# Performance work log

Measured on AMD Instinct MI355X. Metric: run time of the kernel, lower is better.

## Reference

```python
import jax, jax.numpy as jnp
import numpy as np

BITS = 4
QMAX = (1 << BITS) - 1      # 15
QHALF = 1 << (BITS - 1)     # 8
B, S = 4, 2048
IN, OUT, FP = 4096, 4096, 256
INT = IN - FP


def setup_inputs() -> dict:
    key = jax.random.key(0)
    k0, k1, k2, k3 = jax.random.split(key, 4)
    x = jax.random.normal(k0, (B, S, IN), dtype=jnp.float16)
    # disjoint outlier / int feature index sets (QUIK splits columns by outlier-ness)
    perm = np.random.default_rng(0).permutation(IN)
    fp_indices = jnp.sort(jnp.asarray(perm[:FP], dtype=jnp.int32))
    int_indices = jnp.sort(jnp.asarray(perm[FP:], dtype=jnp.int32))
    # unpacked int4 weight values in [-8, 7] (torch stores these packed 2-per-uint8)
    int_weight = jax.random.randint(k1, (OUT, INT), -QHALF, QHALF, dtype=jnp.int8)
    weights_scales = (jax.random.uniform(k2, (OUT, 1), dtype=jnp.float32) * 0.01 + 1e-3).astype(jnp.float16)
    fp_weight = (jax.random.normal(k3, (OUT, FP), dtype=jnp.float32) * 0.02).astype(jnp.float16)
    bias = jnp.zeros((OUT,), dtype=jnp.float16)
    # reduced_w[j] = w_scale[j] * sum_k int_weight[j, k]  (precomputed zero-point correction)
    reduced_w = (weights_scales.astype(jnp.float32)[:, 0] * jnp.sum(int_weight.astype(jnp.float32), axis=1)).reshape(1, OUT).astype(jnp.float16)
    return {"x": x, "int_weight": int_weight, "fp_weight": fp_weight, "bias": bias,
            "weights_scales": weights_scales, "reduced_w": reduced_w,
            "int_indices": int_indices, "fp_indices": fp_indices}


def reference(x, int_weight, fp_weight, bias, weights_scales, reduced_w, int_indices, fp_indices):
    b, s, in_feat = x.shape
    xf = x.reshape(-1, in_feat)                       # [N, in] tokens
    int_x = xf[:, int_indices].astype(jnp.float32)    # [N, INT]
    fp_x = xf[:, fp_indices].astype(jnp.float32)      # [N, FP] outliers stay fp16-precision
    # asymmetric per-token quantization (quik.asymmetric.quantize)
    mn = jnp.min(int_x, axis=1, keepdims=True)
    mx = jnp.max(int_x, axis=1, keepdims=True)
    scale = jnp.maximum((mx - mn) / QMAX, 1e-8)       # [N,1]
    q = (jnp.clip(jnp.round((int_x - mn) / scale), 0, QMAX) - QHALF).astype(jnp.int8)  # signed int4 in [-8,7]
    zero = scale * QHALF + mn                         # [N,1] shifted zero point
    # int4 GEMM (quik.matmul.int4Matmul), int32 accumulate
    int_res = jnp.einsum('nk,ok->no', q, int_weight, preferred_element_type=jnp.int32)
    # fp outlier branch fused with bias (F.linear)
    fp_res = fp_x @ fp_weight.astype(jnp.float32).T + bias.astype(jnp.float32)[None, :]
    # quik.asymmetric.dequantize: q*scale_x*scale_w + zero_x*reduced_w + fp_result
    out = (int_res.astype(jnp.float32) * scale * weights_scales.astype(jnp.float32)[:, 0][None, :]
           + zero * reduced_w.astype(jnp.float32) + fp_res)
    return out.astype(jnp.float16).reshape(b, s, -1)
```

## Files before the change

kernel.cpp:

```cpp
#include <hip/hip_runtime.h>
#include <hip/hip_bf16.h>
#include <stdint.h>

#define N_TOK 8192
#define IN_F  4096
#define OUT_F 4096
#define FP_F  256
#define INT_F 3840
#define PROW  1920

typedef int    v4i   __attribute__((ext_vector_type(4)));
typedef int    v16i  __attribute__((ext_vector_type(16)));
typedef float  v16f  __attribute__((ext_vector_type(16)));
typedef __bf16 bf16x8 __attribute__((ext_vector_type(8)));

#define WS_QP   0u
#define WS_WP   15728640u
#define WS_FPX  23592960u
#define WS_WFP  27787264u
#define WS_F1   29884416u
#define WS_F2   29917184u
#define WS_F3   29949952u
#define WS_NEED 29982720u


__global__ __launch_bounds__(256) void zero_out_kernel(uint4* __restrict__ o) {
  o[(size_t)blockIdx.x * 256 + threadIdx.x] = uint4{0, 0, 0, 0};
}

__global__ __launch_bounds__(256) void prep_kernel(
    const float* __restrict__ x,
    const int* __restrict__ int_idx, const int* __restrict__ fp_idx,
    const int* __restrict__ int_w, const float* __restrict__ fp_w,
    uint8_t* __restrict__ qp, uint8_t* __restrict__ wp,
    __hip_bfloat16* __restrict__ fpx, __hip_bfloat16* __restrict__ wfp,
    float* __restrict__ f1, float* __restrict__ f2, float* __restrict__ f3) {
  __shared__ uint2 qb[240];
  __shared__ float smn[4], smx[4], ssum[4];
  __shared__ float s_mn, s_inv, s_sc;

  int tid = threadIdx.x;
  int blk = blockIdx.x;

  if (blk >= N_TOK) {
    int pb = blk - N_TOK;
    if (pb < OUT_F * 480 / 256) {
      int t = pb * 256 + tid;
      int r = t / 480, u = t % 480;
      int g = u >> 1, h = u & 1;
      const int* src = int_w + (size_t)r * INT_F + g * 16 + h * 4;
      int4 lo = *(const int4*)src;
      int4 hi = *(const int4*)(src + 8);
      uint32_t o = (uint32_t)((lo.x + 8) & 15) | (uint32_t)((hi.x + 8) & 15) << 4 |
                   (uint32_t)((lo.y + 8) & 15) << 8 | (uint32_t)((hi.y + 8) & 15) << 12 |
                   (uint32_t)((lo.z + 8) & 15) << 16 | (uint32_t)((hi.z + 8) & 15) << 20 |
                   (uint32_t)((lo.w + 8) & 15) << 24 | (uint32_t)((hi.w + 8) & 15) << 28;
      int gs = (g & ~7) | ((g & 7) ^ ((r >> 1) & 7));
      ((uint32_t*)wp)[(size_t)r * 480 + gs * 2 + h] = o;
    } else {
      int t = (pb - OUT_F * 480 / 256) * 256 + tid;
      int i = t * 4;
      int r = i >> 8, c = i & 255;
      float4 v = *(const float4*)(fp_w + i);
      __hip_bfloat16 b[4] = {__float2bfloat16(v.x), __float2bfloat16(v.y),
                             __float2bfloat16(v.z), __float2bfloat16(v.w)};
      int cs = (c & ~0x18) | (((((c) >> 3) & 3) ^ ((r >> 1) & 3)) << 3);
      *(uint2*)(wfp + (size_t)r * 256 + cs) = *(const uint2*)b;
    }
    return;
  }

  int n = blk;
  const float* xr = x + (size_t)n * IN_F;

  float v[15];
  float lmn = 1e30f, lmx = -1e30f;
#pragma unroll
  for (int k = 0; k < 15; k++) {
    v[k] = xr[int_idx[tid + 256 * k]];
    lmn = fminf(lmn, v[k]);
    lmx = fmaxf(lmx, v[k]);
  }
  {
    int sw2 = (n >> 1) & 3;
    int cs = (tid & ~0x18) | ((((tid >> 3) & 3) ^ sw2) << 3);
    fpx[(size_t)n * FP_F + cs] = __float2bfloat16(xr[fp_idx[tid]]);
  }

#pragma unroll
  for (int off = 32; off > 0; off >>= 1) {
    lmn = fminf(lmn, __shfl_xor(lmn, off, 64));
    lmx = fmaxf(lmx, __shfl_xor(lmx, off, 64));
  }
  int wv = tid >> 6, ln = tid & 63;
  if (ln == 0) { smn[wv] = lmn; smx[wv] = lmx; }
  __syncthreads();
  if (tid == 0) {
    float mn = fminf(fminf(smn[0], smn[1]), fminf(smn[2], smn[3]));
    float mx = fmaxf(fmaxf(smx[0], smx[1]), fmaxf(smx[2], smx[3]));
    float sc = fmaxf((mx - mn) / 15.0f, 1e-8f);
    s_mn = mn; s_sc = sc; s_inv = 1.0f / sc;
    f1[n] = sc; f3[n] = mn;
  }
  __syncthreads();
  float mn = s_mn, inv = s_inv;

  uint8_t* qbb = (uint8_t*)qb;
  int swq = (n >> 1) & 7;
  float lsum = 0.0f;
#pragma unroll
  for (int k = 0; k < 15; k++) {
    float c = fminf(fmaxf(rintf((v[k] - mn) * inv), 0.0f), 15.0f);
    lsum += c;
    float ch = __shfl_down(c, 8, 64);
    if ((tid & 15) < 8) {
      int G = (tid >> 4) + 16 * k;
      int pos = ((G & ~7) | ((G & 7) ^ swq)) * 8 + (tid & 7);
      qbb[pos] = (uint8_t)((uint32_t)c | ((uint32_t)ch << 4));
    }
  }
#pragma unroll
  for (int off = 32; off > 0; off >>= 1) lsum += __shfl_xor(lsum, off, 64);
  if (ln == 0) ssum[wv] = lsum;
  __syncthreads();
  if (tid == 0)
    f2[n] = -8.0f * (ssum[0] + ssum[1] + ssum[2] + ssum[3]) * s_sc;
  if (tid < 240)
    *(uint2*)(qp + (size_t)n * PROW + tid * 8) = qb[tid];
}

__device__ inline v4i unpack_nib(uint2 u) {
  v4i r;
  r[0] = (int)(u.x & 0x0F0F0F0Fu);
  r[1] = (int)(u.y & 0x0F0F0F0Fu);
  r[2] = (int)((u.x >> 4) & 0x0F0F0F0Fu);
  r[3] = (int)((u.y >> 4) & 0x0F0F0F0Fu);
  return r;
}

__device__ __forceinline__ void gl16(const void* g, void* l) {
  __builtin_amdgcn_global_load_lds(
      (const __attribute__((address_space(1))) void*)g,
      (__attribute__((address_space(3))) void*)l, 16, 0, 0);
}

__global__ __launch_bounds__(256, 4) void gemm_kernel(
    const uint8_t* __restrict__ qp, const uint8_t* __restrict__ wp,
    const __hip_bfloat16* __restrict__ fpx, const __hip_bfloat16* __restrict__ wfp,
    const float* __restrict__ f1, const float* __restrict__ f2,
    const float* __restrict__ f3,
    const float* __restrict__ wscale, const float* __restrict__ reduced,
    const float* __restrict__ bias, float* __restrict__ out) {
  __shared__ int4 lds4[2048];
  int8_t* lds = (int8_t*)lds4;

  int tid = threadIdx.x;
  int wave = tid >> 6, lane = tid & 63;
  int wm = wave >> 1, wn = wave & 1;
  int blk = blockIdx.x;
  int tileM = ((blk & 7) << 3) | ((blk >> 3) & 7);
  int tileN = blk >> 6;
  int n0 = tileM * 128, o0 = tileN * 128;

  union { v16i i; v16f f; } acc[2][2];
#pragma unroll
  for (int mi = 0; mi < 2; mi++)
#pragma unroll
    for (int ni = 0; ni < 2; ni++)
#pragma unroll
      for (int e = 0; e < 16; e++) acc[mi][ni].i[e] = 0;

  int m = lane & 31, kg = lane >> 5;

  int row0 = tid >> 2, q16 = (tid & 3) * 16;
  int l0 = tid * 16, l1 = 4096 + tid * 16;
  const uint8_t* gA0 = qp + (size_t)(n0 + row0) * PROW + q16;
  const uint8_t* gA1 = qp + (size_t)(n0 + 64 + row0) * PROW + q16;
  const uint8_t* gB0 = wp + (size_t)(o0 + row0) * PROW + q16;
  const uint8_t* gB1 = wp + (size_t)(o0 + 64 + row0) * PROW + q16;

#define STAGE_INT(buf, kt) do {                                  \
    gl16(gA0 + (kt) * 64, lds + (buf) * 16384 + l0);             \
    gl16(gA1 + (kt) * 64, lds + (buf) * 16384 + l1);             \
    gl16(gB0 + (kt) * 64, lds + (buf) * 16384 + 8192 + l0);      \
    gl16(gB1 + (kt) * 64, lds + (buf) * 16384 + 8192 + l1);      \
  } while (0)

  auto compute_int = [&](const int8_t* lb) {
#pragma unroll
    for (int ks = 0; ks < 4; ks++) {
      int s8 = ks * 2 + kg;
      v4i a[2], b[2];
#pragma unroll
      for (int mi = 0; mi < 2; mi++) {
        int row = wm * 64 + mi * 32 + m;
        a[mi] = unpack_nib(*(const uint2*)&lb[row * 64 + ((s8 ^ ((row >> 1) & 7)) * 8)]);
      }
#pragma unroll
      for (int ni = 0; ni < 2; ni++) {
        int row = wn * 64 + ni * 32 + m;
        b[ni] = unpack_nib(*(const uint2*)&lb[8192 + row * 64 + ((s8 ^ ((row >> 1) & 7)) * 8)]);
      }
#pragma unroll
      for (int mi = 0; mi < 2; mi++)
#pragma unroll
        for (int ni = 0; ni < 2; ni++)
          acc[mi][ni].i = __builtin_amdgcn_mfma_i32_32x32x32_i8(
              a[mi], b[ni], acc[mi][ni].i, 0, 0, 0);
    }
  };

  STAGE_INT(0, 0);
#pragma unroll 1
  for (int kt = 0; kt < 30; kt += 2) {
    STAGE_INT(1, kt + 1);
    asm volatile("s_waitcnt vmcnt(4)" ::: "memory");
    __builtin_amdgcn_s_barrier();
    compute_int(lds);
    __builtin_amdgcn_s_barrier();
    if (kt + 2 < 30) {
      STAGE_INT(0, kt + 2);
      asm volatile("s_waitcnt vmcnt(4)" ::: "memory");
    } else {
      asm volatile("s_waitcnt vmcnt(0)" ::: "memory");
    }
    __builtin_amdgcn_s_barrier();
    compute_int(lds + 16384);
    __builtin_amdgcn_s_barrier();
  }

  const uint8_t* fxb = (const uint8_t*)fpx;
  const uint8_t* fwb = (const uint8_t*)wfp;
  const uint8_t* gFA0 = fxb + (size_t)(n0 + row0) * 512 + q16;
  const uint8_t* gFA1 = fxb + (size_t)(n0 + 64 + row0) * 512 + q16;
  const uint8_t* gFB0 = fwb + (size_t)(o0 + row0) * 512 + q16;
  const uint8_t* gFB1 = fwb + (size_t)(o0 + 64 + row0) * 512 + q16;

#define STAGE_BF(buf, kr) do {                                   \
    gl16(gFA0 + (kr) * 64, lds + (buf) * 16384 + l0);            \
    gl16(gFA1 + (kr) * 64, lds + (buf) * 16384 + l1);            \
    gl16(gFB0 + (kr) * 64, lds + (buf) * 16384 + 8192 + l0);     \
    gl16(gFB1 + (kr) * 64, lds + (buf) * 16384 + 8192 + l1);     \
  } while (0)

  STAGE_BF(0, 0);

  int col = lane & 31, rb4 = (lane >> 5) * 4;
  float cws[2], crw[2], cbs[2];
#pragma unroll
  for (int ni = 0; ni < 2; ni++) {
    int o = o0 + wn * 64 + ni * 32 + col;
    cws[ni] = wscale[o]; crw[ni] = reduced[o]; cbs[ni] = bias[o];
  }
#pragma unroll
  for (int mi = 0; mi < 2; mi++) {
#pragma unroll
    for (int reg = 0; reg < 16; reg++) {
      int row = (reg & 3) + 8 * (reg >> 2) + rb4;
      int n = n0 + wm * 64 + mi * 32 + row;
      float a1 = f1[n], a2 = f2[n], a3 = f3[n];
      float d0 = (float)acc[mi][0].i[reg];
      float d1 = (float)acc[mi][1].i[reg];
      acc[mi][0].f[reg] = (d0 * a1 + a2) * cws[0] + a3 * crw[0] + cbs[0];
      acc[mi][1].f[reg] = (d1 * a1 + a2) * cws[1] + a3 * crw[1] + cbs[1];
    }
  }

  auto compute_bf = [&](const int8_t* lb) {
#pragma unroll
    for (int kstep = 0; kstep < 2; kstep++) {
      int s16 = kstep * 2 + kg;
      bf16x8 a[2], b[2];
#pragma unroll
      for (int mi = 0; mi < 2; mi++) {
        int row = wm * 64 + mi * 32 + m;
        a[mi] = *(const bf16x8*)&lb[row * 64 + ((s16 ^ ((row >> 1) & 3)) * 16)];
      }
#pragma unroll
      for (int ni = 0; ni < 2; ni++) {
        int row = wn * 64 + ni * 32 + m;
        b[ni] = *(const bf16x8*)&lb[8192 + row * 64 + ((s16 ^ ((row >> 1) & 3)) * 16)];
      }
#pragma unroll
      for (int mi = 0; mi < 2; mi++)
#pragma unroll
        for (int ni = 0; ni < 2; ni++)
          acc[mi][ni].f = __builtin_amdgcn_mfma_f32_32x32x16_bf16(
              a[mi], b[ni], acc[mi][ni].f, 0, 0, 0);
    }
  };

#pragma unroll 1
  for (int kr = 0; kr < 8; kr += 2) {
    STAGE_BF(1, kr + 1);
    asm volatile("s_waitcnt vmcnt(4)" ::: "memory");
    __builtin_amdgcn_s_barrier();
    compute_bf(lds);
    __builtin_amdgcn_s_barrier();
    if (kr + 2 < 8) {
      STAGE_BF(0, kr + 2);
      asm volatile("s_waitcnt vmcnt(4)" ::: "memory");
    } else {
      asm volatile("s_waitcnt vmcnt(0)" ::: "memory");
    }
    __builtin_amdgcn_s_barrier();
    compute_bf(lds + 16384);
    __builtin_amdgcn_s_barrier();
  }

#pragma unroll
  for (int mi = 0; mi < 2; mi++) {
#pragma unroll
    for (int ni = 0; ni < 2; ni++) {
      int o = o0 + wn * 64 + ni * 32 + col;
#pragma unroll
      for (int reg = 0; reg < 16; reg++) {
        int row = (reg & 3) + 8 * (reg >> 2) + rb4;
        int n = n0 + wm * 64 + mi * 32 + row;
        out[(size_t)n * OUT_F + o] = acc[mi][ni].f[reg];
      }
    }
  }
#undef STAGE_INT
#undef STAGE_BF
}

extern "C" void kernel_launch(void* const* d_in, const int* in_sizes, int n_in,
                              void* d_out, int out_size, void* d_ws, size_t ws_size,
                              hipStream_t stream) {
  const float* x     = (const float*)d_in[0];
  const int*   int_w = (const int*)d_in[1];
  const float* fp_w  = (const float*)d_in[2];
  const float* bias  = (const float*)d_in[3];
  const float* wsc   = (const float*)d_in[4];
  const float* red   = (const float*)d_in[5];
  const int*   iidx  = (const int*)d_in[6];
  const int*   fidx  = (const int*)d_in[7];
  float*       out   = (float*)d_out;

  if (ws_size < (size_t)WS_NEED) {
    zero_out_kernel<<<out_size / 1024, 256, 0, stream>>>((uint4*)d_out);
    return;
  }

  uint8_t* ws = (uint8_t*)d_ws;
  uint8_t*        qp  = ws + WS_QP;
  uint8_t*        wpk = ws + WS_WP;
  __hip_bfloat16* fpx = (__hip_bfloat16*)(ws + WS_FPX);
  __hip_bfloat16* wfp = (__hip_bfloat16*)(ws + WS_WFP);
  float*          f1  = (float*)(ws + WS_F1);
  float*          f2  = (float*)(ws + WS_F2);
  float*          f3  = (float*)(ws + WS_F3);

  prep_kernel<<<N_TOK + OUT_F * 480 / 256 + OUT_F * FP_F / 4 / 256, 256, 0, stream>>>(
      x, iidx, fidx, int_w, fp_w, qp, wpk, fpx, wfp, f1, f2, f3);
  gemm_kernel<<<(N_TOK / 128) * (OUT_F / 128), 256, 0, stream>>>(
      qp, wpk, fpx, wfp, f1, f2, f3, wsc, red, bias, out);
}
```

Baseline: 405.2 us.

## Triple-buffer int GEMM loads and use one wave per token in prep

New measurement: 406.7 us. Within noise of the previous version (+0.4%).

```diff
diff --git a/kernel.cpp b/kernel.cpp
--- a/kernel.cpp
+++ b/kernel.cpp
@@ -28,23 +28,21 @@
   o[(size_t)blockIdx.x * 256 + threadIdx.x] = uint4{0, 0, 0, 0};
 }
 
-__global__ __launch_bounds__(256) void prep_kernel(
+__global__ __launch_bounds__(256, 4) void prep_kernel(
     const float* __restrict__ x,
     const int* __restrict__ int_idx, const int* __restrict__ fp_idx,
     const int* __restrict__ int_w, const float* __restrict__ fp_w,
     uint8_t* __restrict__ qp, uint8_t* __restrict__ wp,
     __hip_bfloat16* __restrict__ fpx, __hip_bfloat16* __restrict__ wfp,
     float* __restrict__ f1, float* __restrict__ f2, float* __restrict__ f3) {
-  __shared__ uint2 qb[240];
-  __shared__ float smn[4], smx[4], ssum[4];
-  __shared__ float s_mn, s_inv, s_sc;
+  __shared__ uint2 qb[960];
 
   int tid = threadIdx.x;
   int blk = blockIdx.x;
 
-  if (blk >= N_TOK) {
-    int pb = blk - N_TOK;
-    if (pb < OUT_F * 480 / 256) {
+  if (blk >= 2048) {
+    int pb = blk - 2048;
+    if (pb < 7680) {
       int t = pb * 256 + tid;
       int r = t / 480, u = t % 480;
       int g = u >> 1, h = u & 1;
@@ -58,7 +56,7 @@
       int gs = (g & ~7) | ((g & 7) ^ ((r >> 1) & 7));
       ((uint32_t*)wp)[(size_t)r * 480 + gs * 2 + h] = o;
     } else {
-      int t = (pb - OUT_F * 480 / 256) * 256 + tid;
+      int t = (pb - 7680) * 256 + tid;
       int i = t * 4;
       int r = i >> 8, c = i & 255;
       float4 v = *(const float4*)(fp_w + i);
@@ -70,21 +68,26 @@
     return;
   }
 
-  int n = blk;
+  int wave = tid >> 6, l = tid & 63;
+  int n = blk * 4 + wave;
   const float* xr = x + (size_t)n * IN_F;
 
-  float v[15];
+  float v[60];
   float lmn = 1e30f, lmx = -1e30f;
 #pragma unroll
-  for (int k = 0; k < 15; k++) {
-    v[k] = xr[int_idx[tid + 256 * k]];
+  for (int k = 0; k < 60; k++) {
+    v[k] = xr[int_idx[l + 64 * k]];
     lmn = fminf(lmn, v[k]);
     lmx = fmaxf(lmx, v[k]);
   }
   {
     int sw2 = (n >> 1) & 3;
-    int cs = (tid & ~0x18) | ((((tid >> 3) & 3) ^ sw2) << 3);
-    fpx[(size_t)n * FP_F + cs] = __float2bfloat16(xr[fp_idx[tid]]);
+#pragma unroll
+    for (int j = 0; j < 4; j++) {
+      int c = l + 64 * j;
+      int cs = (c & ~0x18) | ((((c >> 3) & 3) ^ sw2) << 3);
+      fpx[(size_t)n * FP_F + cs] = __float2bfloat16(xr[fp_idx[c]]);
+    }
   }
 
 #pragma unroll
@@ -92,41 +95,35 @@
     lmn = fminf(lmn, __shfl_xor(lmn, off, 64));
     lmx = fmaxf(lmx, __shfl_xor(lmx, off, 64));
   }
-  int wv = tid >> 6, ln = tid & 63;
-  if (ln == 0) { smn[wv] = lmn; smx[wv] = lmx; }
-  __syncthreads();
-  if (tid == 0) {
-    float mn = fminf(fminf(smn[0], smn[1]), fminf(smn[2], smn[3]));
-    float mx = fmaxf(fmaxf(smx[0], smx[1]), fmaxf(smx[2], smx[3]));
-    float sc = fmaxf((mx - mn) / 15.0f, 1e-8f);
-    s_mn = mn; s_sc = sc; s_inv = 1.0f / sc;
-    f1[n] = sc; f3[n] = mn;
-  }
-  __syncthreads();
-  float mn = s_mn, inv = s_inv;
-
-  uint8_t* qbb = (uint8_t*)qb;
+  float mn = lmn;
+  float sc = fmaxf((lmx - mn) / 15.0f, 1e-8f);
+  float inv = 1.0f / sc;
+  if (l == 0) { f1[n] = sc; f3[n] = mn; }
+
+  uint8_t* qbw = (uint8_t*)qb + wave * 1920;
   int swq = (n >> 1) & 7;
   float lsum = 0.0f;
 #pragma unroll
-  for (int k = 0; k < 15; k++) {
+  for (int k = 0; k < 60; k++) {
     float c = fminf(fmaxf(rintf((v[k] - mn) * inv), 0.0f), 15.0f);
     lsum += c;
     float ch = __shfl_down(c, 8, 64);
-    if ((tid & 15) < 8) {
-      int G = (tid >> 4) + 16 * k;
-      int pos = ((G & ~7) | ((G & 7) ^ swq)) * 8 + (tid & 7);
-      qbb[pos] = (uint8_t)((uint32_t)c | ((uint32_t)ch << 4));
+    if ((l & 15) < 8) {
+      int G = (l >> 4) + 4 * k;
+      int pos = ((G & ~7) | ((G & 7) ^ swq)) * 8 + (l & 7);
+      qbw[pos] = (uint8_t)((uint32_t)c | ((uint32_t)ch << 4));
     }
   }
 #pragma unroll
   for (int off = 32; off > 0; off >>= 1) lsum += __shfl_xor(lsum, off, 64);
-  if (ln == 0) ssum[wv] = lsum;
-  __syncthreads();
-  if (tid == 0)
-    f2[n] = -8.0f * (ssum[0] + ssum[1] + ssum[2] + ssum[3]) * s_sc;
-  if (tid < 240)
-    *(uint2*)(qp + (size_t)n * PROW + tid * 8) = qb[tid];
+  if (l == 0) f2[n] = -8.0f * lsum * sc;
+
+  const uint2* qbu = qb + wave * 240;
+#pragma unroll
+  for (int r = 0; r < 4; r++) {
+    int i = l + 64 * r;
+    if (i < 240) *(uint2*)(qp + (size_t)n * PROW + i * 8) = qbu[i];
+  }
 }
 
 __device__ inline v4i unpack_nib(uint2 u) {
@@ -144,14 +141,14 @@
       (__attribute__((address_space(3))) void*)l, 16, 0, 0);
 }
 
-__global__ __launch_bounds__(256, 4) void gemm_kernel(
+__global__ __launch_bounds__(256, 3) void gemm_kernel(
     const uint8_t* __restrict__ qp, const uint8_t* __restrict__ wp,
     const __hip_bfloat16* __restrict__ fpx, const __hip_bfloat16* __restrict__ wfp,
     const float* __restrict__ f1, const float* __restrict__ f2,
     const float* __restrict__ f3,
     const float* __restrict__ wscale, const float* __restrict__ reduced,
     const float* __restrict__ bias, float* __restrict__ out) {
-  __shared__ int4 lds4[2048];
+  __shared__ int4 lds4[3072];
   int8_t* lds = (int8_t*)lds4;
 
   int tid = threadIdx.x;
@@ -172,18 +169,18 @@
 
   int m = lane & 31, kg = lane >> 5;
 
-  int row0 = tid >> 2, q16 = (tid & 3) * 16;
+  int row0 = tid >> 2, q16b = (tid & 3) * 16;
   int l0 = tid * 16, l1 = 4096 + tid * 16;
-  const uint8_t* gA0 = qp + (size_t)(n0 + row0) * PROW + q16;
-  const uint8_t* gA1 = qp + (size_t)(n0 + 64 + row0) * PROW + q16;
-  const uint8_t* gB0 = wp + (size_t)(o0 + row0) * PROW + q16;
-  const uint8_t* gB1 = wp + (size_t)(o0 + 64 + row0) * PROW + q16;
-
-#define STAGE_INT(buf, kt) do {                                  \
-    gl16(gA0 + (kt) * 64, lds + (buf) * 16384 + l0);             \
-    gl16(gA1 + (kt) * 64, lds + (buf) * 16384 + l1);             \
-    gl16(gB0 + (kt) * 64, lds + (buf) * 16384 + 8192 + l0);      \
-    gl16(gB1 + (kt) * 64, lds + (buf) * 16384 + 8192 + l1);      \
+  const uint8_t* gA0 = qp + (size_t)(n0 + row0) * PROW + q16b;
+  const uint8_t* gA1 = qp + (size_t)(n0 + 64 + row0) * PROW + q16b;
+  const uint8_t* gB0 = wp + (size_t)(o0 + row0) * PROW + q16b;
+  const uint8_t* gB1 = wp + (size_t)(o0 + 64 + row0) * PROW + q16b;
+
+#define STAGE_INT(base, kt) do {                                 \
+    gl16(gA0 + (kt) * 64, lds + (base) + l0);                    \
+    gl16(gA1 + (kt) * 64, lds + (base) + l1);                    \
+    gl16(gB0 + (kt) * 64, lds + (base) + 8192 + l0);             \
+    gl16(gB1 + (kt) * 64, lds + (base) + 8192 + l1);             \
   } while (0)
 
   auto compute_int = [&](const int8_t* lb) {
@@ -211,36 +208,37 @@
   };
 
   STAGE_INT(0, 0);
+  STAGE_INT(16384, 1);
+  int rb = 0, sb = 32768;
 #pragma unroll 1
-  for (int kt = 0; kt < 30; kt += 2) {
-    STAGE_INT(1, kt + 1);
-    asm volatile("s_waitcnt vmcnt(4)" ::: "memory");
-    __builtin_amdgcn_s_barrier();
-    compute_int(lds);
-    __builtin_amdgcn_s_barrier();
-    if (kt + 2 < 30) {
-      STAGE_INT(0, kt + 2);
+  for (int t = 0; t < 30; t++) {
+    if (t < 28) {
+      STAGE_INT(sb, t + 2);
+      asm volatile("s_waitcnt vmcnt(8)" ::: "memory");
+    } else if (t == 28) {
       asm volatile("s_waitcnt vmcnt(4)" ::: "memory");
     } else {
       asm volatile("s_waitcnt vmcnt(0)" ::: "memory");
     }
     __builtin_amdgcn_s_barrier();
-    compute_int(lds + 16384);
-    __builtin_amdgcn_s_barrier();
+    compute_int(lds + rb);
+    __builtin_amdgcn_s_barrier();
+    sb = rb;
+    rb = (rb == 32768) ? 0 : rb + 16384;
   }
 
   const uint8_t* fxb = (const uint8_t*)fpx;
   const uint8_t* fwb = (const uint8_t*)wfp;
-  const uint8_t* gFA0 = fxb + (size_t)(n0 + row0) * 512 + q16;
-  const uint8_t* gFA1 = fxb + (size_t)(n0 + 64 + row0) * 512 + q16;
-  const uint8_t* gFB0 = fwb + (size_t)(o0 + row0) * 512 + q16;
-  const uint8_t* gFB1 = fwb + (size_t)(o0 + 64 + row0) * 512 + q16;
-
-#define STAGE_BF(buf, kr) do {                                   \
-    gl16(gFA0 + (kr) * 64, lds + (buf) * 16384 + l0);            \
-    gl16(gFA1 + (kr) * 64, lds + (buf) * 16384 + l1);            \
-    gl16(gFB0 + (kr) * 64, lds + (buf) * 16384 + 8192 + l0);     \
-    gl16(gFB1 + (kr) * 64, lds + (buf) * 16384 + 8192 + l1);     \
+  const uint8_t* gFA0 = fxb + (size_t)(n0 + row0) * 512 + q16b;
+  const uint8_t* gFA1 = fxb + (size_t)(n0 + 64 + row0) * 512 + q16b;
+  const uint8_t* gFB0 = fwb + (size_t)(o0 + row0) * 512 + q16b;
+  const uint8_t* gFB1 = fwb + (size_t)(o0 + 64 + row0) * 512 + q16b;
+
+#define STAGE_BF(base, kr) do {                                  \
+    gl16(gFA0 + (kr) * 64, lds + (base) + l0);                   \
+    gl16(gFA1 + (kr) * 64, lds + (base) + l1);                   \
+    gl16(gFB0 + (kr) * 64, lds + (base) + 8192 + l0);            \
+    gl16(gFB1 + (kr) * 64, lds + (base) + 8192 + l1);            \
   } while (0)
 
   STAGE_BF(0, 0);
@@ -265,6 +263,8 @@
       acc[mi][1].f[reg] = (d1 * a1 + a2) * cws[1] + a3 * crw[1] + cbs[1];
     }
   }
+  asm volatile("s_waitcnt vmcnt(0)" ::: "memory");
+  __builtin_amdgcn_s_barrier();
 
   auto compute_bf = [&](const int8_t* lb) {
 #pragma unroll
@@ -292,7 +292,7 @@
 
 #pragma unroll 1
   for (int kr = 0; kr < 8; kr += 2) {
-    STAGE_BF(1, kr + 1);
+    STAGE_BF(16384, kr + 1);
     asm volatile("s_waitcnt vmcnt(4)" ::: "memory");
     __builtin_amdgcn_s_barrier();
     compute_bf(lds);
@@ -307,6 +307,8 @@
     compute_bf(lds + 16384);
     __builtin_amdgcn_s_barrier();
   }
+#undef STAGE_INT
+#undef STAGE_BF
 
 #pragma unroll
   for (int mi = 0; mi < 2; mi++) {
@@ -321,8 +323,6 @@
       }
     }
   }
-#undef STAGE_INT
-#undef STAGE_BF
 }
 
 extern "C" void kernel_launch(void* const* d_in, const int* in_sizes, int n_in,
@@ -352,7 +352,7 @@
   float*          f2  = (float*)(ws + WS_F2);
   float*          f3  = (float*)(ws + WS_F3);
 
-  prep_kernel<<<N_TOK + OUT_F * 480 / 256 + OUT_F * FP_F / 4 / 256, 256, 0, stream>>>(
+  prep_kernel<<<2048 + 7680 + 1024, 256, 0, stream>>>(
       x, iidx, fidx, int_w, fp_w, qp, wpk, fpx, wfp, f1, f2, f3);
   gemm_kernel<<<(N_TOK / 128) * (OUT_F / 128), 256, 0, stream>>>(
       qp, wpk, fpx, wfp, f1, f2, f3, wsc, red, bias, out);
```
